# Kernel tuning notes

Hardware: AMD Instinct MI355X
Metric: run time of the kernel (lower is better)

Reference implementation:

```python
import jax, jax.numpy as jnp
import numpy as np

N_NODES = 50000
N_EDGES = 800000
IN_DIM, HID_DIM, OUT_DIM = 128, 128, 256


def _gcn_conv(x, W, b, src, dst, num_nodes):
    # PyG GCNConv: h = D^{-1/2} (A + I) D^{-1/2} X W + b (self-loops already in src/dst)
    h = x @ W  # (N, F_out)
    ones = jnp.ones(src.shape[0], dtype=h.dtype)
    deg = jax.ops.segment_sum(ones, dst, num_segments=num_nodes)
    dinv = jnp.where(deg > 0, jax.lax.rsqrt(deg), 0.0)
    norm = dinv[src] * dinv[dst]  # (E,)
    msg = h[src] * norm[:, None]  # (E, F_out) gather
    out = jax.ops.segment_sum(msg, dst, num_segments=num_nodes)  # scatter-add
    return out + b


def setup_inputs() -> dict:
    key = jax.random.key(0)
    ks = jax.random.split(key, 6)
    x = jax.random.normal(ks[0], (N_NODES, IN_DIM), dtype=jnp.float32)
    edge_index = jax.random.randint(ks[1], (2, N_EDGES), 0, N_NODES, dtype=jnp.int64)
    W1 = jax.random.normal(ks[2], (IN_DIM, HID_DIM), dtype=jnp.float32) / np.sqrt(IN_DIM)
    b1 = jnp.zeros((HID_DIM,), jnp.float32)
    W2 = jax.random.normal(ks[3], (HID_DIM, OUT_DIM), dtype=jnp.float32) / np.sqrt(HID_DIM)
    b2 = jnp.zeros((OUT_DIM,), jnp.float32)
    Wa = jax.random.normal(ks[4], (OUT_DIM, 1), dtype=jnp.float32) / np.sqrt(OUT_DIM)
    ba = jnp.zeros((1,), jnp.float32)
    return {"x": x, "edge_index": edge_index, "W1": W1, "b1": b1, "W2": W2, "b2": b2, "Wa": Wa, "ba": ba}


def reference(x, edge_index, W1, b1, W2, b2, Wa, ba):
    n = x.shape[0]
    loops = jnp.arange(n, dtype=edge_index.dtype)
    src = jnp.concatenate([edge_index[0], loops])
    dst = jnp.concatenate([edge_index[1], loops])
    h = jax.nn.relu(_gcn_conv(x, W1, b1, src, dst, n))
    # dropout is a no-op in eval mode
    node_embeddings = jax.nn.relu(_gcn_conv(h, W2, b2, src, dst, n))
    logits = node_embeddings @ Wa + ba  # (N, 1)
    attn = jax.nn.softmax(logits, axis=0)  # softmax over nodes
    graph_embedding = jnp.sum(node_embeddings * attn, axis=0, keepdims=True)  # (1, OUT_DIM)
    return (node_embeddings, graph_embedding)
```

## Files before the change

kernel.cpp:

```cpp
#include <hip/hip_runtime.h>
#include <hip/hip_fp16.h>
#include <math.h>

typedef __attribute__((ext_vector_type(8))) short bf16x8;
typedef __attribute__((ext_vector_type(4))) float f32x4;

static __device__ __forceinline__ unsigned short f2bf(float x) {
    unsigned u = __float_as_uint(x);
    unsigned r = (u + 0x7FFF + ((u >> 16) & 1)) >> 16;
    return (unsigned short)r;
}
static __device__ __forceinline__ float bf2f(unsigned short h) {
    return __uint_as_float(((unsigned)h) << 16);
}
static __device__ __forceinline__ void addh8(float* a, uint4 v) {
    float2 f;
    f = __half22float2(*(const __half2*)&v.x); a[0] += f.x; a[1] += f.y;
    f = __half22float2(*(const __half2*)&v.y); a[2] += f.x; a[3] += f.y;
    f = __half22float2(*(const __half2*)&v.z); a[4] += f.x; a[5] += f.y;
    f = __half22float2(*(const __half2*)&v.w); a[6] += f.x; a[7] += f.y;
}


__global__ __launch_bounds__(256) void count_deg_kernel(const int* __restrict__ dst, int E,
                                                        int* __restrict__ deg,
                                                        int* __restrict__ epos) {
    int e = blockIdx.x * 256 + threadIdx.x;
    if (e < E) epos[e] = atomicAdd(&deg[dst[e]], 1);
}

__global__ __launch_bounds__(256) void scan_partial_kernel(const int* __restrict__ deg, int n,
                                                           int* __restrict__ partials) {
    int idx = blockIdx.x * 1024 + threadIdx.x * 4;
    int4 v = make_int4(0, 0, 0, 0);
    if (idx + 3 < n) v = *(const int4*)(deg + idx);
    else {
        if (idx < n) v.x = deg[idx];
        if (idx + 1 < n) v.y = deg[idx + 1];
        if (idx + 2 < n) v.z = deg[idx + 2];
    }
    int s = v.x + v.y + v.z + v.w;
    for (int off = 1; off < 64; off <<= 1) s += __shfl_xor(s, off);
    __shared__ int sm[4];
    int wave = threadIdx.x >> 6;
    if ((threadIdx.x & 63) == 0) sm[wave] = s;
    __syncthreads();
    if (threadIdx.x == 0) partials[blockIdx.x] = sm[0] + sm[1] + sm[2] + sm[3];
}

__global__ __launch_bounds__(256) void scan_final_kernel(const int* __restrict__ deg, int n,
                                                         const int* __restrict__ partials, int nbk,
                                                         int* __restrict__ rowptr) {
    int idx = blockIdx.x * 1024 + threadIdx.x * 4;
    int4 v = make_int4(0, 0, 0, 0);
    if (idx + 3 < n) v = *(const int4*)(deg + idx);
    else {
        if (idx < n) v.x = deg[idx];
        if (idx + 1 < n) v.y = deg[idx + 1];
        if (idx + 2 < n) v.z = deg[idx + 2];
    }
    int tsum = v.x + v.y + v.z + v.w;
    int lane = threadIdx.x & 63, wave = threadIdx.x >> 6;
    int s = tsum;
    for (int off = 1; off < 64; off <<= 1) {
        int u = __shfl_up(s, off);
        if (lane >= off) s += u;
    }
    __shared__ int wsum[4];
    __shared__ int bb;
    if (lane == 63) wsum[wave] = s;
    if (threadIdx.x < 64) {
        int pv = (threadIdx.x < nbk) ? partials[threadIdx.x] : 0;
        int ps = pv;
        for (int off = 1; off < 64; off <<= 1) {
            int u = __shfl_up(ps, off);
            if (threadIdx.x >= off) ps += u;
        }
        if (threadIdx.x == blockIdx.x) bb = ps - pv;
        if (blockIdx.x == 0 && threadIdx.x == 63) rowptr[n] = ps;
    }
    __syncthreads();
    int base = bb;
    for (int w = 0; w < wave; ++w) base += wsum[w];
    int e0 = base + s - tsum;
    int4 o;
    o.x = e0; o.y = e0 + v.x; o.z = o.y + v.y; o.w = o.z + v.z;
    if (idx + 3 < n) *(int4*)(rowptr + idx) = o;
    else {
        if (idx < n) rowptr[idx] = o.x;
        if (idx + 1 < n) rowptr[idx + 1] = o.y;
        if (idx + 2 < n) rowptr[idx + 2] = o.z;
    }
}


__global__ __launch_bounds__(256) void prep_kernel(
    const int* __restrict__ src, const int* __restrict__ dst, const int* __restrict__ epos, int E,
    const int* __restrict__ rowptr, int* __restrict__ csrsrc, int scatterBlocks,
    const float* __restrict__ x, float* __restrict__ dinv,
    __half2* __restrict__ xs16, int n, int prescaleBlocks,
    const float* __restrict__ W1, const float* __restrict__ W2,
    unsigned short* __restrict__ w1h, unsigned short* __restrict__ w1l,
    unsigned short* __restrict__ w2h, unsigned short* __restrict__ w2l) {
    int b = blockIdx.x;
    if (b < scatterBlocks) {
        int e = b * 256 + threadIdx.x;
        if (e < E) csrsrc[rowptr[dst[e]] + epos[e]] = src[e];
    } else if (b < scatterBlocks + prescaleBlocks) {
        int node = (b - scatterBlocks) * 4 + (threadIdx.x >> 6);
        int lane = threadIdx.x & 63;
        if (node >= n) return;
        float di = rsqrtf((float)(rowptr[node + 1] - rowptr[node] + 1));
        if (lane == 0) dinv[node] = di;
        float2 v = *(const float2*)(x + (size_t)node * 128 + (lane << 1));
        xs16[(size_t)node * 64 + lane] = __floats2half2_rn(di * v.x, di * v.y);
    } else {
        int i = (b - scatterBlocks - prescaleBlocks) * 256 + threadIdx.x;
        if (i < 128 * 128) {
            int nn = i >> 7, k = i & 127;
            float v = W1[k * 128 + nn];
            unsigned short h = f2bf(v);
            w1h[nn * 128 + k] = h;
            w1l[nn * 128 + k] = f2bf(v - bf2f(h));
        } else if (i < 128 * 128 + 256 * 128) {
            int j = i - 128 * 128;
            int nn = j >> 7, k = j & 127;
            float v = W2[k * 256 + nn];
            unsigned short h = f2bf(v);
            w2h[nn * 128 + k] = h;
            w2l[nn * 128 + k] = f2bf(v - bf2f(h));
        }
    }
}


template <int NCOLS, bool SCALE_DINV, bool DO_LOGITS, bool OUT_F16>
__global__ __launch_bounds__(512, 4) void fused_gemm(
    const unsigned short* __restrict__ X16,
    const int* __restrict__ rowptr, const int* __restrict__ csrsrc,
    const float* __restrict__ dinv,
    const unsigned short* __restrict__ Bth, const unsigned short* __restrict__ Btl,
    const float* __restrict__ bias, void* __restrict__ Cout, int M,
    const float* __restrict__ Wa, float* __restrict__ logits) {
    constexpr int CT = NCOLS / 32;
    __shared__ unsigned short AsH[64 * 128];
    __shared__ unsigned short AsL[64 * 128];

    const int t = threadIdx.x;
    const int row0 = blockIdx.x * 64;

    {
        const int nl = t >> 3;
        const int sub = t & 7;
        const int row = row0 + nl;
        float acc[16];
#pragma unroll
        for (int i = 0; i < 16; ++i) acc[i] = 0.f;
        float di = 0.f;
        if (row < M) {
            const uint4* __restrict__ Xv = (const uint4*)X16;
            size_t sb = (size_t)row * 16 + sub * 2;
            uint4 v0 = Xv[sb], v1 = Xv[sb + 1];
            addh8(acc, v0); addh8(acc + 8, v1);
            int e1 = rowptr[row + 1];
            int e = rowptr[row];
            for (; e + 4 <= e1; e += 4) {
                int s0 = csrsrc[e], s1 = csrsrc[e + 1], s2 = csrsrc[e + 2], s3 = csrsrc[e + 3];
                size_t b0 = (size_t)s0 * 16 + sub * 2;
                size_t b1 = (size_t)s1 * 16 + sub * 2;
                size_t b2 = (size_t)s2 * 16 + sub * 2;
                size_t b3 = (size_t)s3 * 16 + sub * 2;
                uint4 a0 = Xv[b0], a1 = Xv[b0 + 1];
                uint4 c0 = Xv[b1], c1 = Xv[b1 + 1];
                uint4 d0 = Xv[b2], d1 = Xv[b2 + 1];
                uint4 f0 = Xv[b3], f1 = Xv[b3 + 1];
                addh8(acc, a0); addh8(acc + 8, a1);
                addh8(acc, c0); addh8(acc + 8, c1);
                addh8(acc, d0); addh8(acc + 8, d1);
                addh8(acc, f0); addh8(acc + 8, f1);
            }
            for (; e < e1; ++e) {
                size_t b0 = (size_t)csrsrc[e] * 16 + sub * 2;
                uint4 a0 = Xv[b0], a1 = Xv[b0 + 1];
                addh8(acc, a0); addh8(acc + 8, a1);
            }
            di = dinv[row];
        }
#pragma unroll
        for (int j = 0; j < 2; ++j) {
            int ga = sub * 2 + j;
            int off = nl * 128 + (ga >> 3) * 64 + (((ga & 7) ^ (nl & 7)) << 3);
            unsigned short h[8], l[8];
#pragma unroll
            for (int q = 0; q < 8; ++q) {
                float f = di * acc[j * 8 + q];
                h[q] = f2bf(f);
                l[q] = f2bf(f - bf2f(h[q]));
            }
            uint4 hv, lv;
            hv.x = (unsigned)h[0] | ((unsigned)h[1] << 16);
            hv.y = (unsigned)h[2] | ((unsigned)h[3] << 16);
            hv.z = (unsigned)h[4] | ((unsigned)h[5] << 16);
            hv.w = (unsigned)h[6] | ((unsigned)h[7] << 16);
            lv.x = (unsigned)l[0] | ((unsigned)l[1] << 16);
            lv.y = (unsigned)l[2] | ((unsigned)l[3] << 16);
            lv.z = (unsigned)l[4] | ((unsigned)l[5] << 16);
            lv.w = (unsigned)l[6] | ((unsigned)l[7] << 16);
            *(uint4*)(AsH + off) = hv;
            *(uint4*)(AsL + off) = lv;
        }
    }
    __syncthreads();

    const int lane = t & 63;
    const int wave = t >> 6;
    const int wrow = wave & 3;
    const int wcol = wave >> 2;
    const int lq = lane >> 4;
    const int lm = lane & 15;

    f32x4 acc2[CT] = {};
    float lacc[4] = {0.f, 0.f, 0.f, 0.f};

#pragma unroll
    for (int kc = 0; kc < 2; ++kc)
#pragma unroll
        for (int ks = 0; ks < 2; ++ks) {
            const int gbase = ks * 4 + lq;
            const int ra = wrow * 16 + lm;
            const int aoff = ra * 128 + kc * 64 + ((gbase ^ (ra & 7)) << 3);
            bf16x8 ah = *(const bf16x8*)(AsH + aoff);
            bf16x8 al = *(const bf16x8*)(AsL + aoff);
#pragma unroll
            for (int ct = 0; ct < CT; ++ct) {
                int col = wcol * (NCOLS / 2) + ct * 16 + lm;
                size_t bo = (size_t)col * 128 + kc * 64 + gbase * 8;
                bf16x8 bh = *(const bf16x8*)(Bth + bo);
                bf16x8 bl = *(const bf16x8*)(Btl + bo);
                acc2[ct] = __builtin_amdgcn_mfma_f32_16x16x32_bf16(ah, bh, acc2[ct], 0, 0, 0);
                acc2[ct] = __builtin_amdgcn_mfma_f32_16x16x32_bf16(al, bh, acc2[ct], 0, 0, 0);
                acc2[ct] = __builtin_amdgcn_mfma_f32_16x16x32_bf16(ah, bl, acc2[ct], 0, 0, 0);
            }
        }

#pragma unroll
    for (int ct = 0; ct < CT; ++ct) {
        int col = wcol * (NCOLS / 2) + ct * 16 + lm;
        float bc = bias[col];
        float wac = DO_LOGITS ? Wa[col] : 0.f;
        int rowb = row0 + wrow * 16 + lq * 4;
#pragma unroll
        for (int reg = 0; reg < 4; ++reg) {
            int gr = rowb + reg;
            if (gr < M) {
                float o = fmaxf(acc2[ct][reg] + bc, 0.f);
                if (SCALE_DINV) o *= dinv[gr];
                if (OUT_F16) ((__half*)Cout)[(size_t)gr * NCOLS + col] = __float2half(o);
                else ((float*)Cout)[(size_t)gr * NCOLS + col] = o;
                if (DO_LOGITS) lacc[reg] += o * wac;
            }
        }
    }

    if (DO_LOGITS) {
#pragma unroll
        for (int reg = 0; reg < 4; ++reg) {
            float s = lacc[reg];
            s += __shfl_xor(s, 1);
            s += __shfl_xor(s, 2);
            s += __shfl_xor(s, 4);
            s += __shfl_xor(s, 8);
            int gr = row0 + wrow * 16 + lq * 4 + reg;
            if (lm == 0 && gr < M) atomicAdd(&logits[gr], s);
        }
    }
}


__global__ __launch_bounds__(256) void maxsum_kernel(const float* __restrict__ logits, int n,
                                                     float2* __restrict__ part,
                                                     float* __restrict__ outTail) {
    if (blockIdx.x == 0) outTail[threadIdx.x] = 0.f;
    float m = -INFINITY, s = 0.f;
    for (int i = blockIdx.x * 256 + threadIdx.x; i < n; i += gridDim.x * 256) {
        float v = logits[i];
        if (v > m) { s = s * expf(m - v) + 1.f; m = v; }
        else s += expf(v - m);
    }
    __shared__ float sm[256], ss[256];
    sm[threadIdx.x] = m; ss[threadIdx.x] = s;
    __syncthreads();
    for (int off = 128; off > 0; off >>= 1) {
        if (threadIdx.x < off) {
            float m1 = sm[threadIdx.x], s1 = ss[threadIdx.x];
            float m2 = sm[threadIdx.x + off], s2 = ss[threadIdx.x + off];
            float M = fmaxf(m1, m2);
            sm[threadIdx.x] = M;
            ss[threadIdx.x] = s1 * expf(m1 - M) + s2 * expf(m2 - M);
        }
        __syncthreads();
    }
    if (threadIdx.x == 0) part[blockIdx.x] = make_float2(sm[0], ss[0]);
}

static __device__ __forceinline__ float2 merge_part(const float2* __restrict__ part, int t,
                                                    float* red2) {
    if (t < 64) {
        float2 p = part[t];
        float m = p.x, s = p.y;
        for (int off = 32; off > 0; off >>= 1) {
            float m2 = __shfl_xor(m, off);
            float s2 = __shfl_xor(s, off);
            float M = fmaxf(m, m2);
            s = s * expf(m - M) + s2 * expf(m2 - M);
            m = M;
        }
        if (t == 0) { red2[0] = m; red2[1] = s; }
    }
    __syncthreads();
    return make_float2(red2[0], red2[1]);
}

__global__ __launch_bounds__(256) void weighted_sum_kernel(const float* __restrict__ emb,
                                                           const float* __restrict__ logits,
                                                           const float2* __restrict__ part,
                                                           float* __restrict__ gpart, int n) {
    __shared__ float red2[2];
    float g = merge_part(part, threadIdx.x, red2).x;
    int wave = threadIdx.x >> 6;
    int lane = threadIdx.x & 63;
    int stride = gridDim.x * 4;
    float4 acc = make_float4(0.f, 0.f, 0.f, 0.f);
#pragma unroll 2
    for (int r = blockIdx.x * 4 + wave; r < n; r += stride) {
        float w = expf(logits[r] - g);
        float4 v = *(const float4*)(emb + (size_t)r * 256 + (lane << 2));
        acc.x += w * v.x; acc.y += w * v.y; acc.z += w * v.z; acc.w += w * v.w;
    }
    __shared__ float4 sm[256];
    sm[threadIdx.x] = acc;
    __syncthreads();
    if (wave == 0) {
        float4 a = sm[lane], b = sm[64 + lane], c = sm[128 + lane], d = sm[192 + lane];
        float4 s;
        s.x = (a.x + b.x) + (c.x + d.x);
        s.y = (a.y + b.y) + (c.y + d.y);
        s.z = (a.z + b.z) + (c.z + d.z);
        s.w = (a.w + b.w) + (c.w + d.w);
        *(float4*)(gpart + (size_t)blockIdx.x * 256 + (lane << 2)) = s;
    }
}

__global__ __launch_bounds__(256) void reduce_gpart_kernel(const float* __restrict__ gpart,
                                                           const float2* __restrict__ part,
                                                           float* __restrict__ outTail, int nb) {
    __shared__ float red2[2];
    float gsum = merge_part(part, threadIdx.x, red2).y;
    int rows = nb / gridDim.x;
    int r0 = blockIdx.x * rows;
    float s = 0.f;
    for (int r = r0; r < r0 + rows; ++r) s += gpart[(size_t)r * 256 + threadIdx.x];
    atomicAdd(&outTail[threadIdx.x], s / gsum);
}


extern "C" void kernel_launch(void* const* d_in, const int* in_sizes, int n_in,
                              void* d_out, int out_size, void* d_ws, size_t ws_size,
                              hipStream_t stream) {
    const float* x  = (const float*)d_in[0];
    const int* ei   = (const int*)d_in[1];
    const float* W1 = (const float*)d_in[2];
    const float* b1 = (const float*)d_in[3];
    const float* W2 = (const float*)d_in[4];
    const float* b2 = (const float*)d_in[5];
    const float* Wa = (const float*)d_in[6];
    float* out = (float*)d_out;

    const int n = in_sizes[0] / 128;
    const int E = in_sizes[1] / 2;
    const int* srcA = ei;
    const int* dstA = ei + E;
    const int nb = (n + 1023) / 1024;
    const int WS_BLOCKS = 1024;

    unsigned short* xs16 = (unsigned short*)d_ws;
    unsigned short* h16  = xs16 + (size_t)n * 128;
    unsigned short* w1h  = h16 + (size_t)n * 128;
    unsigned short* w1l  = w1h + 128 * 128;
    unsigned short* w2h  = w1l + 128 * 128;
    unsigned short* w2l  = w2h + 256 * 128;
    float* dinv   = (float*)(w2l + 256 * 128);
    float* logits = dinv + n;
    int* deg      = (int*)(logits + n);
    int* rowptr   = deg + n;
    int* partials = rowptr + n + 1;
    float2* part  = (float2*)(partials + 64);
    float* gpart  = (float*)(part + 64);
    int* epos     = (int*)(gpart + WS_BLOCKS * 256);
    int* csrsrc   = epos + E;

    hipMemsetAsync(logits, 0, sizeof(float) * (size_t)(2 * n), stream);

    count_deg_kernel<<<(E + 255) / 256, 256, 0, stream>>>(dstA, E, deg, epos);
    scan_partial_kernel<<<nb, 256, 0, stream>>>(deg, n, partials);
    scan_final_kernel<<<nb, 256, 0, stream>>>(deg, n, partials, nb, rowptr);

    int scatterBlocks = (E + 255) / 256;
    int prescaleBlocks = (n + 3) / 4;
    int wconvBlocks = (128 * 128 + 256 * 128 + 255) / 256;
    prep_kernel<<<scatterBlocks + prescaleBlocks + wconvBlocks, 256, 0, stream>>>(
        srcA, dstA, epos, E, rowptr, csrsrc, scatterBlocks,
        x, dinv, (__half2*)xs16, n, prescaleBlocks,
        W1, W2, w1h, w1l, w2h, w2l);

    int gemmRows = (n + 63) / 64;

    fused_gemm<128, true, false, true><<<gemmRows, 512, 0, stream>>>(
        xs16, rowptr, csrsrc, dinv, w1h, w1l, b1, h16, n, nullptr, nullptr);
    fused_gemm<256, false, true, false><<<gemmRows, 512, 0, stream>>>(
        h16, rowptr, csrsrc, dinv, w2h, w2l, b2, out, n, Wa, logits);

    maxsum_kernel<<<64, 256, 0, stream>>>(logits, n, part, out + (size_t)n * 256);
    weighted_sum_kernel<<<WS_BLOCKS, 256, 0, stream>>>(out, logits, part, gpart, n);
    reduce_gpart_kernel<<<32, 256, 0, stream>>>(gpart, part, out + (size_t)n * 256, WS_BLOCKS);
}
```

Measured before the change: 336.1 us.

## Shrink fused GEMM tile to 16 rows with 16 threads per node gather

The fused aggregate+GEMM kernel now handles 16 rows per block with 256 threads instead of 64 rows with 512 threads. Each node's gather is spread over 16 lanes, each loading one uint4, instead of 8 lanes loading two. The gather loop is unrolled by 8 to keep more loads in flight. Each wave now covers all 16 rows and a quarter of the output columns. The intent is more blocks, smaller LDS use and better latency hiding in the irregular gather. The cost is that B (weight) fragments are reloaded from global or L2 for every 16 rows rather than every 64, roughly quadrupling weight traffic.

```diff
diff --git a/kernel.cpp b/kernel.cpp
--- a/kernel.cpp
+++ b/kernel.cpp
@@ -135,87 +135,80 @@
 
 
 template <int NCOLS, bool SCALE_DINV, bool DO_LOGITS, bool OUT_F16>
-__global__ __launch_bounds__(512, 4) void fused_gemm(
+__global__ __launch_bounds__(256, 4) void fused_gemm(
     const unsigned short* __restrict__ X16,
     const int* __restrict__ rowptr, const int* __restrict__ csrsrc,
     const float* __restrict__ dinv,
     const unsigned short* __restrict__ Bth, const unsigned short* __restrict__ Btl,
     const float* __restrict__ bias, void* __restrict__ Cout, int M,
     const float* __restrict__ Wa, float* __restrict__ logits) {
-    constexpr int CT = NCOLS / 32;
-    __shared__ unsigned short AsH[64 * 128];
-    __shared__ unsigned short AsL[64 * 128];
+    constexpr int CT = NCOLS / 64;
+    __shared__ unsigned short AsH[16 * 128];
+    __shared__ unsigned short AsL[16 * 128];
 
     const int t = threadIdx.x;
-    const int row0 = blockIdx.x * 64;
+    const int row0 = blockIdx.x * 16;
 
     {
-        const int nl = t >> 3;
-        const int sub = t & 7;
+        const int nl = t >> 4;
+        const int sub = t & 15;
         const int row = row0 + nl;
-        float acc[16];
-#pragma unroll
-        for (int i = 0; i < 16; ++i) acc[i] = 0.f;
+        float acc[8] = {0.f, 0.f, 0.f, 0.f, 0.f, 0.f, 0.f, 0.f};
         float di = 0.f;
         if (row < M) {
             const uint4* __restrict__ Xv = (const uint4*)X16;
-            size_t sb = (size_t)row * 16 + sub * 2;
-            uint4 v0 = Xv[sb], v1 = Xv[sb + 1];
-            addh8(acc, v0); addh8(acc + 8, v1);
+            addh8(acc, Xv[(size_t)row * 16 + sub]);
             int e1 = rowptr[row + 1];
             int e = rowptr[row];
+            for (; e + 8 <= e1; e += 8) {
+                int s0 = csrsrc[e], s1 = csrsrc[e + 1], s2 = csrsrc[e + 2], s3 = csrsrc[e + 3];
+                int s4 = csrsrc[e + 4], s5 = csrsrc[e + 5], s6 = csrsrc[e + 6], s7 = csrsrc[e + 7];
+                uint4 v0 = Xv[(size_t)s0 * 16 + sub];
+                uint4 v1 = Xv[(size_t)s1 * 16 + sub];
+                uint4 v2 = Xv[(size_t)s2 * 16 + sub];
+                uint4 v3 = Xv[(size_t)s3 * 16 + sub];
+                uint4 v4 = Xv[(size_t)s4 * 16 + sub];
+                uint4 v5 = Xv[(size_t)s5 * 16 + sub];
+                uint4 v6 = Xv[(size_t)s6 * 16 + sub];
+                uint4 v7 = Xv[(size_t)s7 * 16 + sub];
+                addh8(acc, v0); addh8(acc, v1); addh8(acc, v2); addh8(acc, v3);
+                addh8(acc, v4); addh8(acc, v5); addh8(acc, v6); addh8(acc, v7);
+            }
             for (; e + 4 <= e1; e += 4) {
                 int s0 = csrsrc[e], s1 = csrsrc[e + 1], s2 = csrsrc[e + 2], s3 = csrsrc[e + 3];
-                size_t b0 = (size_t)s0 * 16 + sub * 2;
-                size_t b1 = (size_t)s1 * 16 + sub * 2;
-                size_t b2 = (size_t)s2 * 16 + sub * 2;
-                size_t b3 = (size_t)s3 * 16 + sub * 2;
-                uint4 a0 = Xv[b0], a1 = Xv[b0 + 1];
-                uint4 c0 = Xv[b1], c1 = Xv[b1 + 1];
-                uint4 d0 = Xv[b2], d1 = Xv[b2 + 1];
-                uint4 f0 = Xv[b3], f1 = Xv[b3 + 1];
-                addh8(acc, a0); addh8(acc + 8, a1);
-                addh8(acc, c0); addh8(acc + 8, c1);
-                addh8(acc, d0); addh8(acc + 8, d1);
-                addh8(acc, f0); addh8(acc + 8, f1);
+                uint4 v0 = Xv[(size_t)s0 * 16 + sub];
+                uint4 v1 = Xv[(size_t)s1 * 16 + sub];
+                uint4 v2 = Xv[(size_t)s2 * 16 + sub];
+                uint4 v3 = Xv[(size_t)s3 * 16 + sub];
+                addh8(acc, v0); addh8(acc, v1); addh8(acc, v2); addh8(acc, v3);
             }
-            for (; e < e1; ++e) {
-                size_t b0 = (size_t)csrsrc[e] * 16 + sub * 2;
-                uint4 a0 = Xv[b0], a1 = Xv[b0 + 1];
-                addh8(acc, a0); addh8(acc + 8, a1);
-            }
+            for (; e < e1; ++e) addh8(acc, Xv[(size_t)csrsrc[e] * 16 + sub]);
             di = dinv[row];
         }
-#pragma unroll
-        for (int j = 0; j < 2; ++j) {
-            int ga = sub * 2 + j;
-            int off = nl * 128 + (ga >> 3) * 64 + (((ga & 7) ^ (nl & 7)) << 3);
-            unsigned short h[8], l[8];
-#pragma unroll
-            for (int q = 0; q < 8; ++q) {
-                float f = di * acc[j * 8 + q];
-                h[q] = f2bf(f);
-                l[q] = f2bf(f - bf2f(h[q]));
-            }
-            uint4 hv, lv;
-            hv.x = (unsigned)h[0] | ((unsigned)h[1] << 16);
-            hv.y = (unsigned)h[2] | ((unsigned)h[3] << 16);
-            hv.z = (unsigned)h[4] | ((unsigned)h[5] << 16);
-            hv.w = (unsigned)h[6] | ((unsigned)h[7] << 16);
-            lv.x = (unsigned)l[0] | ((unsigned)l[1] << 16);
-            lv.y = (unsigned)l[2] | ((unsigned)l[3] << 16);
-            lv.z = (unsigned)l[4] | ((unsigned)l[5] << 16);
-            lv.w = (unsigned)l[6] | ((unsigned)l[7] << 16);
-            *(uint4*)(AsH + off) = hv;
-            *(uint4*)(AsL + off) = lv;
-        }
+        int off = nl * 128 + (sub >> 3) * 64 + (((sub & 7) ^ (nl & 7)) << 3);
+        unsigned short h[8], l[8];
+#pragma unroll
+        for (int q = 0; q < 8; ++q) {
+            float f = di * acc[q];
+            h[q] = f2bf(f);
+            l[q] = f2bf(f - bf2f(h[q]));
+        }
+        uint4 hv, lv;
+        hv.x = (unsigned)h[0] | ((unsigned)h[1] << 16);
+        hv.y = (unsigned)h[2] | ((unsigned)h[3] << 16);
+        hv.z = (unsigned)h[4] | ((unsigned)h[5] << 16);
+        hv.w = (unsigned)h[6] | ((unsigned)h[7] << 16);
+        lv.x = (unsigned)l[0] | ((unsigned)l[1] << 16);
+        lv.y = (unsigned)l[2] | ((unsigned)l[3] << 16);
+        lv.z = (unsigned)l[4] | ((unsigned)l[5] << 16);
+        lv.w = (unsigned)l[6] | ((unsigned)l[7] << 16);
+        *(uint4*)(AsH + off) = hv;
+        *(uint4*)(AsL + off) = lv;
     }
     __syncthreads();
 
     const int lane = t & 63;
     const int wave = t >> 6;
-    const int wrow = wave & 3;
-    const int wcol = wave >> 2;
     const int lq = lane >> 4;
     const int lm = lane & 15;
 
@@ -227,13 +220,12 @@
 #pragma unroll
         for (int ks = 0; ks < 2; ++ks) {
             const int gbase = ks * 4 + lq;
-            const int ra = wrow * 16 + lm;
-            const int aoff = ra * 128 + kc * 64 + ((gbase ^ (ra & 7)) << 3);
+            const int aoff = lm * 128 + kc * 64 + ((gbase ^ (lm & 7)) << 3);
             bf16x8 ah = *(const bf16x8*)(AsH + aoff);
             bf16x8 al = *(const bf16x8*)(AsL + aoff);
 #pragma unroll
             for (int ct = 0; ct < CT; ++ct) {
-                int col = wcol * (NCOLS / 2) + ct * 16 + lm;
+                int col = wave * (NCOLS / 4) + ct * 16 + lm;
                 size_t bo = (size_t)col * 128 + kc * 64 + gbase * 8;
                 bf16x8 bh = *(const bf16x8*)(Bth + bo);
                 bf16x8 bl = *(const bf16x8*)(Btl + bo);
@@ -245,10 +237,10 @@
 
 #pragma unroll
     for (int ct = 0; ct < CT; ++ct) {
-        int col = wcol * (NCOLS / 2) + ct * 16 + lm;
+        int col = wave * (NCOLS / 4) + ct * 16 + lm;
         float bc = bias[col];
         float wac = DO_LOGITS ? Wa[col] : 0.f;
-        int rowb = row0 + wrow * 16 + lq * 4;
+        int rowb = row0 + lq * 4;
 #pragma unroll
         for (int reg = 0; reg < 4; ++reg) {
             int gr = rowb + reg;
@@ -270,7 +262,7 @@
             s += __shfl_xor(s, 2);
             s += __shfl_xor(s, 4);
             s += __shfl_xor(s, 8);
-            int gr = row0 + wrow * 16 + lq * 4 + reg;
+            int gr = row0 + lq * 4 + reg;
             if (lm == 0 && gr < M) atomicAdd(&logits[gr], s);
         }
     }
@@ -413,11 +405,11 @@
         x, dinv, (__half2*)xs16, n, prescaleBlocks,
         W1, W2, w1h, w1l, w2h, w2l);
 
-    int gemmRows = (n + 63) / 64;
-
-    fused_gemm<128, true, false, true><<<gemmRows, 512, 0, stream>>>(
+    int gemmRows = (n + 15) / 16;
+
+    fused_gemm<128, true, false, true><<<gemmRows, 256, 0, stream>>>(
         xs16, rowptr, csrsrc, dinv, w1h, w1l, b1, h16, n, nullptr, nullptr);
-    fused_gemm<256, false, true, false><<<gemmRows, 512, 0, stream>>>(
+    fused_gemm<256, false, true, false><<<gemmRows, 256, 0, stream>>>(
         h16, rowptr, csrsrc, dinv, w2h, w2l, b2, out, n, Wa, logits);
 
     maxsum_kernel<<<64, 256, 0, stream>>>(logits, n, part, out + (size_t)n * 256);
```

Result: faster. 322.7 us (-4.0%).
